# Optimization experiments

Hardware: AMD Instinct MI355X
Metric: run time of the kernel (lower is better)

Reference implementation:

```python
import jax, jax.numpy as jnp
import numpy as np

B, S, D, H = 2, 1536, 1024, 16
DK = D // H
NEG = -1e9
WEIGHT = 1.0  # undefined global `Weight` in source; treated as scalar 1.0


def setup_inputs() -> dict:
    key = jax.random.key(0)
    ks = jax.random.split(key, 16)
    inp = {
        "query": jax.random.normal(ks[0], (B, S, D), jnp.float32),
        "key": jax.random.normal(ks[1], (B, S, D), jnp.float32),
        "value": jax.random.normal(ks[2], (B, S, D), jnp.float32),
        "mask": jax.random.randint(ks[3], (B, 1, 1, S), 0, 2, jnp.int32),
        "mask1": jax.random.randint(ks[4], (B, 1, S, S), 0, 2, jnp.int32).astype(jnp.float32),
        "Wq": jax.random.normal(ks[5], (D, D), jnp.float32) / np.sqrt(D),
        "bq": jnp.zeros((D,), jnp.float32),
        "Wk": jax.random.normal(ks[6], (D, D), jnp.float32) / np.sqrt(D),
        "bk": jnp.zeros((D,), jnp.float32),
        "Wv": jax.random.normal(ks[7], (D, D), jnp.float32) / np.sqrt(D),
        "bv": jnp.zeros((D,), jnp.float32),
        "Wo": jax.random.normal(ks[8], (D, D), jnp.float32) / np.sqrt(D),
        "bo": jnp.zeros((D,), jnp.float32),
    }
    return inp


def _split_heads(x):
    # [B,S,D] -> [B,H,S,DK]
    return x.reshape(B, S, H, DK).transpose(0, 2, 1, 3)


def reference(query, key, value, mask, mask1, Wq, bq, Wk, bk, Wv, bv, Wo, bo):
    q = _split_heads(query @ Wq.T + bq)
    k = _split_heads(key @ Wk.T + bk)
    v = _split_heads(value @ Wv.T + bv)

    scores = jnp.einsum("bhqd,bhkd->bhqk", q, k) / jnp.sqrt(jnp.float32(DK))
    # softmax of mask1 over the query axis (dim=-2), zeros masked out
    m1 = jnp.where(mask1 == 0, NEG, mask1)
    m1s = jax.nn.softmax(m1, axis=-2)
    scores = (1.0 + m1s * mask1) * scores * WEIGHT
    scores = jnp.where(mask == 0, NEG, scores)
    p = jax.nn.softmax(scores, axis=-1)  # dropout: eval mode (identity)
    x = jnp.einsum("bhqk,bhkd->bhqd", p, v)
    x = x.transpose(0, 2, 1, 3).reshape(B, S, D)
    ret = x @ Wo.T + bo
    return ret, scores
```

## Files before the change

### kernel.cpp

```cpp
#include <hip/hip_runtime.h>
#include <hip/hip_bf16.h>

#define B_ 2
#define S_ 1536
#define D_ 1024
#define H_ 16
#define DK_ 64
#define KW_ 48
#define NT_ 24

#define RET_ELEMS 3145728
#define BITPACK_BLOCKS 18432

typedef __attribute__((ext_vector_type(8))) short short8;
typedef __attribute__((ext_vector_type(8))) unsigned short ushort8v;
typedef __attribute__((ext_vector_type(4))) unsigned short ushort4v;
typedef __attribute__((ext_vector_type(4))) float f32x4;

__device__ __forceinline__ unsigned short bf16_rne(float f) {
    return __builtin_bit_cast(unsigned short, __float2bfloat16(f));
}

struct CvtJobs {
    const float* src[7];
    unsigned short* dst[7];
};

__global__ __launch_bounds__(256) void preproc_kernel(
    const float* __restrict__ mask1, unsigned int* __restrict__ bits,
    float* __restrict__ colsum, CvtJobs j)
{
    const int blk = blockIdx.x;
    if (blk < BITPACK_BLOCKS) {
        if (blk < 12) colsum[blk * 256 + threadIdx.x] = 0.f;
        const size_t gid = (size_t)blk * 256 + threadIdx.x;
        const float v = mask1[gid];
        const unsigned long long bal = __ballot(v != 0.f);
        const int l = threadIdx.x & 63;
        if (l == 0)       bits[gid >> 5] = (unsigned int)bal;
        else if (l == 32) bits[gid >> 5] = (unsigned int)(bal >> 32);
        return;
    }
    int rb = blk - BITPACK_BLOCKS;
    int job, base;
    if (rb < 4608) { job = rb / 1536; base = rb % 1536; }
    else { rb -= 4608; job = 3 + rb / 512; base = rb % 512; }
    const size_t i = ((size_t)base * 256 + threadIdx.x) * 8;
    const float* s = j.src[job] + i;
    float4 f0 = *(const float4*)s;
    float4 f1 = *(const float4*)(s + 4);
    ushort8v u;
    u[0]=bf16_rne(f0.x); u[1]=bf16_rne(f0.y); u[2]=bf16_rne(f0.z); u[3]=bf16_rne(f0.w);
    u[4]=bf16_rne(f1.x); u[5]=bf16_rne(f1.y); u[6]=bf16_rne(f1.z); u[7]=bf16_rne(f1.w);
    *(ushort8v*)(j.dst[job] + i) = u;
}

__global__ void colcount_bits_kernel(const unsigned int* __restrict__ bits, float* __restrict__ colsum) {
    const int b     = blockIdx.x / 6;
    const int chunk = blockIdx.x % 6;
    const int col   = chunk * 256 + threadIdx.x;
    const int q0    = blockIdx.y * 96;
    const int wword = col >> 5, bit = col & 31;
    const unsigned int* p = bits + ((size_t)b * S_ + q0) * KW_ + wword;
    int s = 0;
    #pragma unroll 8
    for (int q = 0; q < 96; ++q) s += (p[(size_t)q * KW_] >> bit) & 1u;
    atomicAdd(&colsum[b * S_ + col], (float)s);
}

struct Proj { const unsigned short* A; const unsigned short* W; const float* bias; unsigned short* C; };

__global__ __launch_bounds__(512) void qkv_gemm_kernel(Proj p0, Proj p1, Proj p2) {
    const int bid = blockIdx.x;
    const int xcd = bid & 7, idx = bid >> 3;
    const int zy = xcd * 9 + (idx >> 3);
    const int bx = idx & 7;
    const int z = zy / 24, by = zy % 24;

    const unsigned short* A = z == 0 ? p0.A    : (z == 1 ? p1.A    : p2.A);
    const unsigned short* W = z == 0 ? p0.W    : (z == 1 ? p1.W    : p2.W);
    const float* bias       = z == 0 ? p0.bias : (z == 1 ? p1.bias : p2.bias);
    unsigned short* C       = z == 0 ? p0.C    : (z == 1 ? p1.C    : p2.C);

    __shared__ unsigned short As[128][72];
    __shared__ unsigned short Bs[128][72];
    const int tid = threadIdx.x;
    const int w = tid >> 6, lane = tid & 63;
    const int g = lane >> 4, c = lane & 15;
    const int wm = w >> 2, wn = w & 3;
    const int m0 = by * 128, n0 = bx * 128;
    const int trow = tid >> 2;
    const int tcol = (tid & 3) * 16;

    f32x4 acc[4][2];
    #pragma unroll
    for (int m = 0; m < 4; ++m)
        #pragma unroll
        for (int n = 0; n < 2; ++n)
            acc[m][n] = f32x4{0.f, 0.f, 0.f, 0.f};

    for (int k0 = 0; k0 < D_; k0 += 64) {
        {
            const unsigned short* ap = A + (size_t)(m0 + trow) * D_ + k0 + tcol;
            *(ushort8v*)&As[trow][tcol]     = *(const ushort8v*)ap;
            *(ushort8v*)&As[trow][tcol + 8] = *(const ushort8v*)(ap + 8);
            const unsigned short* wp = W + (size_t)(n0 + trow) * D_ + k0 + tcol;
            *(ushort8v*)&Bs[trow][tcol]     = *(const ushort8v*)wp;
            *(ushort8v*)&Bs[trow][tcol + 8] = *(const ushort8v*)(wp + 8);
        }
        __syncthreads();
        #pragma unroll
        for (int kk = 0; kk < 2; ++kk) {
            short8 a[4], bb[2];
            #pragma unroll
            for (int m = 0; m < 4; ++m) a[m]  = *(const short8*)&As[wm * 64 + m * 16 + c][kk * 32 + g * 8];
            #pragma unroll
            for (int n = 0; n < 2; ++n) bb[n] = *(const short8*)&Bs[wn * 32 + n * 16 + c][kk * 32 + g * 8];
            #pragma unroll
            for (int m = 0; m < 4; ++m)
                #pragma unroll
                for (int n = 0; n < 2; ++n)
                    acc[m][n] = __builtin_amdgcn_mfma_f32_16x16x32_bf16(a[m], bb[n], acc[m][n], 0, 0, 0);
        }
        __syncthreads();
    }
    #pragma unroll
    for (int n = 0; n < 2; ++n) {
        const int col = n0 + wn * 32 + n * 16 + c;
        const float bval = bias[col];
        #pragma unroll
        for (int m = 0; m < 4; ++m) {
            const int row0 = m0 + wm * 64 + m * 16 + g * 4;
            #pragma unroll
            for (int r = 0; r < 4; ++r)
                C[(size_t)(row0 + r) * D_ + col] = bf16_rne(acc[m][n][r] + bval);
        }
    }
}

__global__ __launch_bounds__(256) void out_gemm_kernel(
    const unsigned short* __restrict__ A, const unsigned short* __restrict__ W,
    const float* __restrict__ bias, float* __restrict__ C)
{
    const int bid = blockIdx.x;
    const int xcd = bid & 7, idx = bid >> 3;
    const int yg = xcd * 6 + (idx >> 4);
    const int bx = idx & 15;

    __shared__ unsigned short As[64][72];
    __shared__ unsigned short Bs[64][72];
    const int tid = threadIdx.x;
    const int w = tid >> 6, lane = tid & 63;
    const int g = lane >> 4, c = lane & 15;
    const int wm = w >> 1, wn = w & 1;
    const int m0 = yg * 64, n0 = bx * 64;
    const int trow = tid >> 2;
    const int tcol = (tid & 3) * 16;

    f32x4 acc[2][2];
    #pragma unroll
    for (int m = 0; m < 2; ++m)
        #pragma unroll
        for (int n = 0; n < 2; ++n)
            acc[m][n] = f32x4{0.f, 0.f, 0.f, 0.f};

    for (int k0 = 0; k0 < D_; k0 += 64) {
        {
            const unsigned short* ap = A + (size_t)(m0 + trow) * D_ + k0 + tcol;
            *(ushort8v*)&As[trow][tcol]     = *(const ushort8v*)ap;
            *(ushort8v*)&As[trow][tcol + 8] = *(const ushort8v*)(ap + 8);
            const unsigned short* wp = W + (size_t)(n0 + trow) * D_ + k0 + tcol;
            *(ushort8v*)&Bs[trow][tcol]     = *(const ushort8v*)wp;
            *(ushort8v*)&Bs[trow][tcol + 8] = *(const ushort8v*)(wp + 8);
        }
        __syncthreads();
        #pragma unroll
        for (int kk = 0; kk < 2; ++kk) {
            short8 a[2], bb[2];
            #pragma unroll
            for (int m = 0; m < 2; ++m) a[m]  = *(const short8*)&As[wm * 32 + m * 16 + c][kk * 32 + g * 8];
            #pragma unroll
            for (int n = 0; n < 2; ++n) bb[n] = *(const short8*)&Bs[wn * 32 + n * 16 + c][kk * 32 + g * 8];
            #pragma unroll
            for (int m = 0; m < 2; ++m)
                #pragma unroll
                for (int n = 0; n < 2; ++n)
                    acc[m][n] = __builtin_amdgcn_mfma_f32_16x16x32_bf16(a[m], bb[n], acc[m][n], 0, 0, 0);
        }
        __syncthreads();
    }
    #pragma unroll
    for (int n = 0; n < 2; ++n) {
        const int col = n0 + wn * 32 + n * 16 + c;
        const float bval = bias[col];
        #pragma unroll
        for (int m = 0; m < 2; ++m) {
            const int row0 = m0 + wm * 32 + m * 16 + g * 4;
            #pragma unroll
            for (int r = 0; r < 4; ++r)
                C[(size_t)(row0 + r) * D_ + col] = acc[m][n][r] + bval;
        }
    }
}

__global__ __launch_bounds__(256) void attn_kernel(
    const unsigned short* __restrict__ Qb, const unsigned short* __restrict__ Kb,
    const unsigned short* __restrict__ Vb, const int* __restrict__ mask,
    const unsigned int* __restrict__ bits, const float* __restrict__ colsum,
    float* __restrict__ scores, unsigned short* __restrict__ X)
{
    const int bid = blockIdx.x;
    const int xcd = bid & 7, idx = bid >> 3;
    const int grp = xcd * 4 + idx / 24;
    const int qt  = idx % 24;
    const int h = grp & 15, b = grp >> 4;

    const int tid = threadIdx.x;
    const int w = tid >> 6, lane = tid & 63;
    const int g = lane >> 4, c = lane & 15;

    __shared__ unsigned short VT_lds[2][64][72];
    __shared__ unsigned short P_lds[4][16][72];
    __shared__ float fac_lds[S_];

    for (int i = tid; i < S_; i += 256) {
        const int km = mask[b * S_ + i];
        const float cnt = colsum[b * S_ + i];
        fac_lds[i] = (km == 0) ? -1.f : ((cnt > 0.f) ? (1.f / cnt) : 0.f);
    }

    const int qrow0 = qt * 64 + w * 16;
    const unsigned short* qptr = Qb + ((size_t)b * S_ + qrow0 + c) * D_ + h * DK_;
    const short8 qf0 = *(const short8*)(qptr + g * 8);
    const short8 qf1 = *(const short8*)(qptr + 32 + g * 8);

    float mrow = -INFINITY, lrow = 0.f;
    f32x4 o[4];
    #pragma unroll
    for (int n = 0; n < 4; ++n) o[n] = f32x4{0.f, 0.f, 0.f, 0.f};

    float* srow = scores + ((((size_t)(b * H_ + h)) * S_ + qrow0 + c) * S_);
    const unsigned int* brow = bits + ((size_t)b * S_ + qrow0 + c) * KW_;
    const int kr = tid & 63, half = tid >> 6;
    const unsigned short* vrow = Vb + ((size_t)b * S_ + kr) * D_ + h * DK_ + half * 16;

    {
        short8 v0 = *(const short8*)vrow;
        short8 v1 = *(const short8*)(vrow + 8);
        #pragma unroll
        for (int j = 0; j < 8; ++j) {
            VT_lds[0][half * 16 + j][kr]     = (unsigned short)v0[j];
            VT_lds[0][half * 16 + 8 + j][kr] = (unsigned short)v1[j];
        }
    }
    __syncthreads();

    for (int kt = 0; kt < NT_; ++kt) {
        const int k0 = kt * 64;
        const int cur = kt & 1;
        const bool have_next = (kt + 1) < NT_;

        short8 nv0, nv1;
        if (have_next) {
            const unsigned short* vs = vrow + (size_t)(k0 + 64) * D_;
            nv0 = *(const short8*)vs;
            nv1 = *(const short8*)(vs + 8);
        }

        f32x4 sacc[4];
        #pragma unroll
        for (int n = 0; n < 4; ++n) sacc[n] = f32x4{0.f, 0.f, 0.f, 0.f};
        short8 kf0[4], kf1[4];
        #pragma unroll
        for (int n = 0; n < 4; ++n) {
            const unsigned short* kp = Kb + ((size_t)b * S_ + k0 + n * 16 + c) * D_ + h * DK_;
            kf0[n] = *(const short8*)(kp + g * 8);
            kf1[n] = *(const short8*)(kp + 32 + g * 8);
        }
        __builtin_amdgcn_s_setprio(1);
        #pragma unroll
        for (int n = 0; n < 4; ++n) {
            sacc[n] = __builtin_amdgcn_mfma_f32_16x16x32_bf16(kf0[n], qf0, sacc[n], 0, 0, 0);
            sacc[n] = __builtin_amdgcn_mfma_f32_16x16x32_bf16(kf1[n], qf1, sacc[n], 0, 0, 0);
        }
        __builtin_amdgcn_s_setprio(0);

        const unsigned int w0 = brow[(k0 >> 5)];
        const unsigned int w1 = brow[(k0 >> 5) + 1];
        float pmax = -INFINITY;
        f32x4 sv[4];
        #pragma unroll
        for (int n = 0; n < 4; ++n) {
            const f32x4 fv = *(const f32x4*)&fac_lds[k0 + n * 16 + g * 4];
            const unsigned int wsel = (n < 2) ? w0 : w1;
            #pragma unroll
            for (int r = 0; r < 4; ++r) {
                const int kl = n * 16 + g * 4 + r;
                const float f = fv[r];
                const float icnt = fmaxf(f, 0.f);
                const float bit = (float)((wsel >> (kl & 31)) & 1u);
                float s = sacc[n][r] * 0.125f * (1.f + bit * icnt);
                s = (f < 0.f) ? -1e9f : s;
                sv[n][r] = s;
                pmax = fmaxf(pmax, s);
            }
            __builtin_nontemporal_store(sv[n], (f32x4*)&srow[k0 + n * 16 + g * 4]);
        }

        pmax = fmaxf(pmax, __shfl_xor(pmax, 16));
        pmax = fmaxf(pmax, __shfl_xor(pmax, 32));
        const float nm = fmaxf(mrow, pmax);
        const float scq = __expf(mrow - nm);
        mrow = nm;
        lrow *= scq;
        float sc_o[4];
        #pragma unroll
        for (int r = 0; r < 4; ++r) sc_o[r] = __shfl(scq, (lane & 48) | (g * 4 + r));
        #pragma unroll
        for (int n = 0; n < 4; ++n)
            #pragma unroll
            for (int r = 0; r < 4; ++r) o[n][r] *= sc_o[r];

        #pragma unroll
        for (int n = 0; n < 4; ++n) {
            ushort4v pu;
            #pragma unroll
            for (int r = 0; r < 4; ++r) {
                const float p = __expf(sv[n][r] - mrow);
                lrow += p;
                pu[r] = bf16_rne(p);
            }
            *(ushort4v*)&P_lds[w][c][n * 16 + g * 4] = pu;
        }

        if (have_next) {
            #pragma unroll
            for (int j = 0; j < 8; ++j) {
                VT_lds[cur ^ 1][half * 16 + j][kr]     = (unsigned short)nv0[j];
                VT_lds[cur ^ 1][half * 16 + 8 + j][kr] = (unsigned short)nv1[j];
            }
        }

        __builtin_amdgcn_s_setprio(1);
        #pragma unroll
        for (int kk = 0; kk < 2; ++kk) {
            const short8 pa = *(const short8*)&P_lds[w][c][kk * 32 + g * 8];
            #pragma unroll
            for (int n = 0; n < 4; ++n) {
                const short8 vf = *(const short8*)&VT_lds[cur][n * 16 + c][kk * 32 + g * 8];
                o[n] = __builtin_amdgcn_mfma_f32_16x16x32_bf16(pa, vf, o[n], 0, 0, 0);
            }
        }
        __builtin_amdgcn_s_setprio(0);
        __syncthreads();
    }

    lrow += __shfl_xor(lrow, 16);
    lrow += __shfl_xor(lrow, 32);
    const float linv = 1.f / lrow;
    float linv_o[4];
    #pragma unroll
    for (int r = 0; r < 4; ++r) linv_o[r] = __shfl(linv, (lane & 48) | (g * 4 + r));
    #pragma unroll
    for (int n = 0; n < 4; ++n)
        #pragma unroll
        for (int r = 0; r < 4; ++r) {
            const size_t idx2 = ((size_t)b * S_ + qrow0 + g * 4 + r) * D_ + h * DK_ + n * 16 + c;
            X[idx2] = bf16_rne(o[n][r] * linv_o[r]);
        }
}

extern "C" void kernel_launch(void* const* d_in, const int* in_sizes, int n_in,
                              void* d_out, int out_size, void* d_ws, size_t ws_size,
                              hipStream_t stream) {
    const float* query = (const float*)d_in[0];
    const float* key   = (const float*)d_in[1];
    const float* value = (const float*)d_in[2];
    const int*   mask  = (const int*)d_in[3];
    const float* mask1 = (const float*)d_in[4];
    const float* Wq = (const float*)d_in[5];
    const float* bq = (const float*)d_in[6];
    const float* Wk = (const float*)d_in[7];
    const float* bk = (const float*)d_in[8];
    const float* Wv = (const float*)d_in[9];
    const float* bv = (const float*)d_in[10];
    const float* Wo = (const float*)d_in[11];
    const float* bo = (const float*)d_in[12];

    float* ret_out    = (float*)d_out;
    float* scores_out = ret_out + RET_ELEMS;

    const size_t SZ = (size_t)B_ * S_ * D_;
    const size_t WZ = (size_t)D_ * D_;
    float* colsum = (float*)d_ws;
    unsigned int* bits = (unsigned int*)((char*)d_ws + 16384);
    unsigned short* Qb  = (unsigned short*)((char*)d_ws + 16384 + 589824);
    unsigned short* Kb  = Qb + SZ;
    unsigned short* Vb  = Kb + SZ;
    unsigned short* Xb  = Vb + SZ;
    unsigned short* qf  = Xb + SZ;
    unsigned short* kf  = qf + SZ;
    unsigned short* vf  = kf + SZ;
    unsigned short* Wqb = vf + SZ;
    unsigned short* Wkb = Wqb + WZ;
    unsigned short* Wvb = Wkb + WZ;
    unsigned short* Wob = Wvb + WZ;

    CvtJobs jobs;
    jobs.src[0] = query; jobs.dst[0] = qf;
    jobs.src[1] = key;   jobs.dst[1] = kf;
    jobs.src[2] = value; jobs.dst[2] = vf;
    jobs.src[3] = Wq;    jobs.dst[3] = Wqb;
    jobs.src[4] = Wk;    jobs.dst[4] = Wkb;
    jobs.src[5] = Wv;    jobs.dst[5] = Wvb;
    jobs.src[6] = Wo;    jobs.dst[6] = Wob;

    preproc_kernel<<<BITPACK_BLOCKS + 3 * 1536 + 4 * 512, 256, 0, stream>>>(mask1, bits, colsum, jobs);
    colcount_bits_kernel<<<dim3(12, 16), 256, 0, stream>>>(bits, colsum);

    Proj p0{qf, Wqb, bq, Qb}, p1{kf, Wkb, bk, Kb}, p2{vf, Wvb, bv, Vb};
    qkv_gemm_kernel<<<576, 512, 0, stream>>>(p0, p1, p2);

    attn_kernel<<<768, 256, 0, stream>>>(Qb, Kb, Vb, mask, bits, colsum, scores_out, Xb);

    out_gemm_kernel<<<768, 256, 0, stream>>>(Xb, Wob, bo, ret_out);
}
```

Baseline: 201.5 us.

## Halve attention block size and precompute mask factors in a separate kernel

The attention kernel now uses 128-thread blocks covering 32 query rows, launched as 1536 blocks instead of 768. Each thread loads twice as many V elements into the transposed LDS tile. The per-block recomputation of the mask/colsum factor array into LDS moves to a small new kernel that writes it to global memory. This aims to raise occupancy and cut per-block setup and LDS use, at the cost of fewer rows sharing each K/V tile, and therefore more K/V traffic, plus an extra kernel launch.

```diff
diff --git a/kernel.cpp b/kernel.cpp
--- a/kernel.cpp
+++ b/kernel.cpp
@@ -68,6 +68,16 @@
     atomicAdd(&colsum[b * S_ + col], (float)s);
 }
 
+__global__ void fac_kernel(const int* __restrict__ mask, const float* __restrict__ colsum,
+                           float* __restrict__ fac) {
+    const int i = blockIdx.x * 256 + threadIdx.x;
+    if (i < B_ * S_) {
+        const int km = mask[i];
+        const float cnt = colsum[i];
+        fac[i] = (km == 0) ? -1.f : ((cnt > 0.f) ? (1.f / cnt) : 0.f);
+    }
+}
+
 struct Proj { const unsigned short* A; const unsigned short* W; const float* bias; unsigned short* C; };
 
 __global__ __launch_bounds__(512) void qkv_gemm_kernel(Proj p0, Proj p1, Proj p2) {
@@ -203,16 +213,16 @@
     }
 }
 
-__global__ __launch_bounds__(256) void attn_kernel(
+__global__ __launch_bounds__(128) void attn_kernel(
     const unsigned short* __restrict__ Qb, const unsigned short* __restrict__ Kb,
-    const unsigned short* __restrict__ Vb, const int* __restrict__ mask,
-    const unsigned int* __restrict__ bits, const float* __restrict__ colsum,
+    const unsigned short* __restrict__ Vb, const float* __restrict__ fac,
+    const unsigned int* __restrict__ bits,
     float* __restrict__ scores, unsigned short* __restrict__ X)
 {
     const int bid = blockIdx.x;
     const int xcd = bid & 7, idx = bid >> 3;
-    const int grp = xcd * 4 + idx / 24;
-    const int qt  = idx % 24;
+    const int grp = xcd * 4 + idx / 48;
+    const int qt  = idx % 48;
     const int h = grp & 15, b = grp >> 4;
 
     const int tid = threadIdx.x;
@@ -220,16 +230,9 @@
     const int g = lane >> 4, c = lane & 15;
 
     __shared__ unsigned short VT_lds[2][64][72];
-    __shared__ unsigned short P_lds[4][16][72];
-    __shared__ float fac_lds[S_];
-
-    for (int i = tid; i < S_; i += 256) {
-        const int km = mask[b * S_ + i];
-        const float cnt = colsum[b * S_ + i];
-        fac_lds[i] = (km == 0) ? -1.f : ((cnt > 0.f) ? (1.f / cnt) : 0.f);
-    }
-
-    const int qrow0 = qt * 64 + w * 16;
+    __shared__ unsigned short P_lds[2][16][72];
+
+    const int qrow0 = qt * 32 + w * 16;
     const unsigned short* qptr = Qb + ((size_t)b * S_ + qrow0 + c) * D_ + h * DK_;
     const short8 qf0 = *(const short8*)(qptr + g * 8);
     const short8 qf1 = *(const short8*)(qptr + 32 + g * 8);
@@ -241,16 +244,22 @@
 
     float* srow = scores + ((((size_t)(b * H_ + h)) * S_ + qrow0 + c) * S_);
     const unsigned int* brow = bits + ((size_t)b * S_ + qrow0 + c) * KW_;
+    const float* frow = fac + (size_t)b * S_;
+
     const int kr = tid & 63, half = tid >> 6;
-    const unsigned short* vrow = Vb + ((size_t)b * S_ + kr) * D_ + h * DK_ + half * 16;
+    const unsigned short* vrow = Vb + ((size_t)b * S_ + kr) * D_ + h * DK_ + half * 32;
 
     {
         short8 v0 = *(const short8*)vrow;
         short8 v1 = *(const short8*)(vrow + 8);
+        short8 v2 = *(const short8*)(vrow + 16);
+        short8 v3 = *(const short8*)(vrow + 24);
         #pragma unroll
         for (int j = 0; j < 8; ++j) {
-            VT_lds[0][half * 16 + j][kr]     = (unsigned short)v0[j];
-            VT_lds[0][half * 16 + 8 + j][kr] = (unsigned short)v1[j];
+            VT_lds[0][half * 32 + j][kr]      = (unsigned short)v0[j];
+            VT_lds[0][half * 32 + 8 + j][kr]  = (unsigned short)v1[j];
+            VT_lds[0][half * 32 + 16 + j][kr] = (unsigned short)v2[j];
+            VT_lds[0][half * 32 + 24 + j][kr] = (unsigned short)v3[j];
         }
     }
     __syncthreads();
@@ -260,11 +269,13 @@
         const int cur = kt & 1;
         const bool have_next = (kt + 1) < NT_;
 
-        short8 nv0, nv1;
+        short8 nv0, nv1, nv2, nv3;
         if (have_next) {
             const unsigned short* vs = vrow + (size_t)(k0 + 64) * D_;
             nv0 = *(const short8*)vs;
             nv1 = *(const short8*)(vs + 8);
+            nv2 = *(const short8*)(vs + 16);
+            nv3 = *(const short8*)(vs + 24);
         }
 
         f32x4 sacc[4];
@@ -291,7 +302,7 @@
         f32x4 sv[4];
         #pragma unroll
         for (int n = 0; n < 4; ++n) {
-            const f32x4 fv = *(const f32x4*)&fac_lds[k0 + n * 16 + g * 4];
+            const f32x4 fv = *(const f32x4*)&frow[k0 + n * 16 + g * 4];
             const unsigned int wsel = (n < 2) ? w0 : w1;
             #pragma unroll
             for (int r = 0; r < 4; ++r) {
@@ -336,8 +347,10 @@
         if (have_next) {
             #pragma unroll
             for (int j = 0; j < 8; ++j) {
-                VT_lds[cur ^ 1][half * 16 + j][kr]     = (unsigned short)nv0[j];
-                VT_lds[cur ^ 1][half * 16 + 8 + j][kr] = (unsigned short)nv1[j];
+                VT_lds[cur ^ 1][half * 32 + j][kr]      = (unsigned short)nv0[j];
+                VT_lds[cur ^ 1][half * 32 + 8 + j][kr]  = (unsigned short)nv1[j];
+                VT_lds[cur ^ 1][half * 32 + 16 + j][kr] = (unsigned short)nv2[j];
+                VT_lds[cur ^ 1][half * 32 + 24 + j][kr] = (unsigned short)nv3[j];
             }
         }
 
@@ -405,6 +418,7 @@
     unsigned short* Wkb = Wqb + WZ;
     unsigned short* Wvb = Wkb + WZ;
     unsigned short* Wob = Wvb + WZ;
+    float* fac = (float*)(Wob + WZ);
 
     CvtJobs jobs;
     jobs.src[0] = query; jobs.dst[0] = qf;
@@ -417,11 +431,12 @@
 
     preproc_kernel<<<BITPACK_BLOCKS + 3 * 1536 + 4 * 512, 256, 0, stream>>>(mask1, bits, colsum, jobs);
     colcount_bits_kernel<<<dim3(12, 16), 256, 0, stream>>>(bits, colsum);
+    fac_kernel<<<12, 256, 0, stream>>>(mask, colsum, fac);
 
     Proj p0{qf, Wqb, bq, Qb}, p1{kf, Wkb, bk, Kb}, p2{vf, Wvb, bv, Vb};
     qkv_gemm_kernel<<<576, 512, 0, stream>>>(p0, p1, p2);
 
-    attn_kernel<<<768, 256, 0, stream>>>(Qb, Kb, Vb, mask, bits, colsum, scores_out, Xb);
+    attn_kernel<<<1536, 128, 0, stream>>>(Qb, Kb, Vb, fac, bits, scores_out, Xb);
 
     out_gemm_kernel<<<768, 256, 0, stream>>>(Xb, Wob, bo, ret_out);
 }
```

Measured after the change: 219.9 us. +9.1%, slower.
